# Optimization experiments

Measured on AMD Instinct MI355X. Metric: run time of the kernel, lower is better.

Reference implementation:

```python
import jax, jax.numpy as jnp
import numpy as np

B, T, F, U, L = 64, 700, 3, 400, 3


def setup_inputs() -> dict:
    key = jax.random.key(0)
    ks = jax.random.split(key, 10)
    s = 0.08  # small init to keep gates unsaturated
    return {
        "x": jax.random.normal(ks[0], (B, T, F), jnp.float32),
        "Wx0": jax.random.normal(ks[1], (F, 4 * U), jnp.float32) * s,
        "Wx1": jax.random.normal(ks[2], (U, 4 * U), jnp.float32) * s,
        "Wx2": jax.random.normal(ks[3], (U, 4 * U), jnp.float32) * s,
        "Wh": jax.random.normal(ks[4], (L, U, 4 * U), jnp.float32) * s,
        "b": jnp.zeros((L, 4 * U), jnp.float32),
        "pi": jax.random.normal(ks[5], (L, U), jnp.float32) * s,
        "pf": jax.random.normal(ks[6], (L, U), jnp.float32) * s,
        "po": jax.random.normal(ks[7], (L, U), jnp.float32) * s,
        "Wd": jax.random.normal(ks[8], (U, F), jnp.float32) * s,
        "bd": jnp.zeros((F,), jnp.float32),
    }


def _lstm_peephole_layer(x_tbd, Wx, Wh_l, b_l, pi_l, pf_l, po_l):
    """x_tbd: [T, B, D] -> [T, B, U] with peephole LSTM (Graves 2013)."""
    Bsz = x_tbd.shape[1]
    Uu = Wh_l.shape[0]
    # Precompute the input contribution for all timesteps in one GEMM.
    xp = jnp.einsum("tbd,dk->tbk", x_tbd, Wx) + b_l  # [T, B, 4U]

    def step(carry, zt):
        h, c = carry
        z = zt + h @ Wh_l  # [B, 4U]
        zi, zf, zg, zo = jnp.split(z, 4, axis=-1)
        i = jax.nn.sigmoid(zi + pi_l * c)
        f = jax.nn.sigmoid(zf + pf_l * c)
        c_new = f * c + i * jnp.tanh(zg)
        o = jax.nn.sigmoid(zo + po_l * c_new)
        h_new = o * jnp.tanh(c_new)
        return (h_new, c_new), h_new

    init = (jnp.zeros((Bsz, Uu), x_tbd.dtype), jnp.zeros((Bsz, Uu), x_tbd.dtype))
    _, hs = jax.lax.scan(step, init, xp)
    return hs  # [T, B, U]


def reference(x, Wx0, Wx1, Wx2, Wh, b, pi, pf, po, Wd, bd):
    h = jnp.transpose(x, (1, 0, 2))  # [T, B, F]
    for l, Wx in enumerate((Wx0, Wx1, Wx2)):
        h = _lstm_peephole_layer(h, Wx, Wh[l], b[l], pi[l], pf[l], po[l])
    out = jnp.einsum("tbu,uf->tbf", h, Wd) + bd
    return jnp.transpose(out, (1, 0, 2))  # [B, T, F]
```

## Files before the change

kernel.cpp:

```cpp
#include <hip/hip_runtime.h>
#include <hip/hip_fp16.h>
#include <math.h>

#define B_ 64
#define T_ 700
#define U_ 400
#define NF 704
#define CHUNK_DW 256
#define FR_LS 13312

typedef _Float16 half8 __attribute__((ext_vector_type(8)));
typedef float float4v __attribute__((ext_vector_type(4)));

union AFrag { unsigned u[4]; half8 h; };

__device__ __forceinline__ unsigned agloadu(const unsigned* p) {
    return __hip_atomic_load(p, __ATOMIC_RELAXED, __HIP_MEMORY_SCOPE_AGENT);
}
__device__ __forceinline__ void agstoreu(unsigned* p, unsigned v) {
    __hip_atomic_store(p, v, __ATOMIC_RELAXED, __HIP_MEMORY_SCOPE_AGENT);
}
__device__ __forceinline__ float sig_(float v) {
    return __builtin_amdgcn_rcpf(1.f + __expf(-v));
}
__device__ __forceinline__ float tanh_(float v) {
    return 1.f - 2.f * __builtin_amdgcn_rcpf(__expf(2.f * v) + 1.f);
}
__device__ __forceinline__ void waitflag(const unsigned* f, unsigned target) {
    while (agloadu(f) < target) __builtin_amdgcn_s_sleep(2);
}
__device__ __forceinline__ unsigned f16u(float v) {
    union { _Float16 f; unsigned short s; } cv; cv.f = (_Float16)v; return (unsigned)cv.s;
}

template<int DEPTH, int CP>
__global__ void __launch_bounds__(256, 1)
lstm_mfma(const float* __restrict__ x,
          const float* __restrict__ Wx0,
          const float* __restrict__ Wx1,
          const float* __restrict__ Wx2,
          const float* __restrict__ Wh,
          const float* __restrict__ bias,
          const float* __restrict__ pi,
          const float* __restrict__ pf,
          const float* __restrict__ po,
          const float* __restrict__ Wd,
          const float* __restrict__ bd,
          float* __restrict__ out,
          unsigned* __restrict__ ws)
{
    __shared__ alignas(16) _Float16 wlds[26 * 512];
    __shared__ alignas(16) float zlds[4 * 528];
    __shared__ float gc[160];

    const int LW = NF * CP * 32;
    unsigned* F0 = ws;
    unsigned* F1 = F0 + LW;
    unsigned* F2 = F1 + LW;
    unsigned* FO = F2 + LW;
    unsigned* frag0 = ws + (size_t)4 * LW;

    const int blk  = blockIdx.x;
    const int tid  = threadIdx.x;
    const int lane = tid & 63;
    const int wv   = tid >> 6;
    const int cpi  = (blk + wv) & (CP - 1);

    int layer, u0;
    if      (blk < 50)  { layer = 0; u0 = blk * 8; }
    else if (blk < 150) { layer = 1; u0 = (blk - 50) * 4; }
    else if (blk < 250) { layer = 2; u0 = (blk - 150) * 4; }
    else                { layer = 3; u0 = 0; }

    {
        const float* __restrict__ Wxl = (layer == 1) ? Wx1 : Wx2;
        for (int i = tid; i < 26 * 64; i += 256) {
            const int ln = i & 63, ck = i >> 6;
            const int q = ln >> 4, nn = ln & 15;
            float vals[8];
#pragma unroll
            for (int j = 0; j < 8; ++j) {
                const int kc = ck % 13;
                const int k = kc * 32 + q * 8 + j;
                float v = 0.f;
                if (k < 400) {
                    if (layer == 0) {
                        const int col32 = (ck / 13) * 16 + nn;
                        const int gcol = (col32 >> 3) * U_ + u0 + (col32 & 7);
                        v = Wh[(size_t)k * 1600 + gcol];
                    } else if (layer < 3) {
                        const int gcol = (nn >> 2) * U_ + u0 + (nn & 3);
                        v = (ck >= 13) ? Wh[((size_t)layer * U_ + k) * 1600 + gcol]
                                       : Wxl[(size_t)k * 1600 + gcol];
                    } else {
                        if (ck < 13 && nn < 3) v = Wd[k * 3 + nn];
                    }
                }
                vals[j] = v;
            }
#pragma unroll
            for (int j = 0; j < 8; ++j)
                wlds[ck * 512 + ln * 8 + j] = (_Float16)vals[j];
        }
        if (layer == 0) {
            if (tid < 128) {
                const int col32 = tid >> 2, comp = tid & 3;
                const int gcol = (col32 >> 3) * U_ + u0 + (col32 & 7);
                gc[tid] = (comp == 0) ? bias[gcol] : Wx0[(size_t)(comp - 1) * 1600 + gcol];
            } else if (tid < 152) {
                const int idx = tid - 128, ul = idx / 3, j = idx - ul * 3;
                const float* pp = (j == 0) ? pi : (j == 1) ? pf : po;
                gc[tid] = pp[u0 + ul];
            }
        } else if (layer < 3) {
            if (tid < 16) {
                gc[tid] = bias[layer * 1600 + (tid >> 2) * U_ + u0 + (tid & 3)];
            } else if (tid < 28) {
                const int idx = tid - 16, ul = idx / 3, j = idx - ul * 3;
                const float* pp = (j == 0) ? pi : (j == 1) ? pf : po;
                gc[tid] = pp[layer * U_ + u0 + ul];
            }
        } else {
            if (tid < 3) gc[tid] = bd[tid];
        }
    }
    __syncthreads();

    const int wvz   = wv * 528;
    const int b_loc = lane & 15;
    const int quad  = lane >> 4;
    float cst[2] = {0.f, 0.f};

    for (int t = 0; t < T_; ++t) {
        const int sw = t % DEPTH;
        const int sr = (t + DEPTH - 1) % DEPTH;

        float x0, x1, x2;
        if (layer == 0) {
            const size_t xb = (size_t)(wv * 16 + b_loc) * T_ + t;
            x0 = x[xb * 3 + 0]; x1 = x[xb * 3 + 1]; x2 = x[xb * 3 + 2];
        }

        if (lane == 0) {
            if (layer == 0) {
                if (t >= 1) waitflag(F0 + ((t - 1) * CP + cpi) * 32, 50);
                if (wv == 0 && t >= DEPTH) waitflag(F1 + ((t - DEPTH) * CP + cpi) * 32, 100);
            } else if (layer == 1) {
                if (t >= 1) waitflag(F1 + ((t - 1) * CP + cpi) * 32, 100);
            } else if (layer == 2) {
                if (t >= 1) waitflag(F2 + ((t - 1) * CP + cpi) * 32, 100);
            } else {
                waitflag(F2 + (t * CP + cpi) * 32, 100);
            }
        }
        asm volatile("" ::: "memory");

        AFrag aown[13];
        {
            const unsigned* fr = (layer == 3)
                ? frag0 + ((size_t)(2 * DEPTH + sw)) * FR_LS + wv * 3328
                : frag0 + ((size_t)(layer * DEPTH + sr)) * FR_LS + wv * 3328;
#pragma unroll
            for (int kc = 0; kc < 13; ++kc)
#pragma unroll
                for (int d = 0; d < 4; ++d)
                    aown[kc].u[d] = agloadu(fr + kc * 256 + d * 64 + lane);
        }

        AFrag ainp[13];
        if (layer == 1 || layer == 2) {
            if (lane == 0) {
                if (layer == 1) {
                    waitflag(F0 + (t * CP + cpi) * 32, 50);
                    if (wv == 0 && t >= DEPTH) waitflag(F2 + ((t - DEPTH) * CP + cpi) * 32, 100);
                } else {
                    waitflag(F1 + (t * CP + cpi) * 32, 100);
                    if (wv == 0 && t >= DEPTH) waitflag(FO + ((t - DEPTH) * CP + cpi) * 32, 1);
                }
            }
            asm volatile("" ::: "memory");
            const unsigned* fr = frag0 + ((size_t)((layer - 1) * DEPTH + sw)) * FR_LS + wv * 3328;
#pragma unroll
            for (int kc = 0; kc < 13; ++kc)
#pragma unroll
                for (int d = 0; d < 4; ++d)
                    ainp[kc].u[d] = agloadu(fr + kc * 256 + d * 64 + lane);
        }

        if (layer == 0) {
            float4v acc0 = {0.f, 0.f, 0.f, 0.f}, acc1 = {0.f, 0.f, 0.f, 0.f};
#pragma unroll
            for (int kc = 0; kc < 13; ++kc) {
                const half8 w0 = *(const half8*)&wlds[kc * 512 + lane * 8];
                const half8 w1 = *(const half8*)&wlds[(13 + kc) * 512 + lane * 8];
                acc0 = __builtin_amdgcn_mfma_f32_16x16x32_f16(aown[kc].h, w0, acc0, 0, 0, 0);
                acc1 = __builtin_amdgcn_mfma_f32_16x16x32_f16(aown[kc].h, w1, acc1, 0, 0, 0);
            }
#pragma unroll
            for (int r = 0; r < 4; ++r) {
                zlds[wvz + (quad * 4 + r) * 33 + b_loc] = acc0[r];
                zlds[wvz + (quad * 4 + r) * 33 + 16 + b_loc] = acc1[r];
            }
        } else if (layer < 3) {
            float4v acc = {0.f, 0.f, 0.f, 0.f};
#pragma unroll
            for (int kc = 0; kc < 13; ++kc) {
                const half8 wA = *(const half8*)&wlds[kc * 512 + lane * 8];
                const half8 wB = *(const half8*)&wlds[(13 + kc) * 512 + lane * 8];
                acc = __builtin_amdgcn_mfma_f32_16x16x32_f16(ainp[kc].h, wA, acc, 0, 0, 0);
                acc = __builtin_amdgcn_mfma_f32_16x16x32_f16(aown[kc].h, wB, acc, 0, 0, 0);
            }
#pragma unroll
            for (int r = 0; r < 4; ++r)
                zlds[wvz + (quad * 4 + r) * 33 + b_loc] = acc[r];
        } else {
            float4v acc = {0.f, 0.f, 0.f, 0.f};
#pragma unroll
            for (int kc = 0; kc < 13; ++kc) {
                const half8 w0 = *(const half8*)&wlds[kc * 512 + lane * 8];
                acc = __builtin_amdgcn_mfma_f32_16x16x32_f16(aown[kc].h, w0, acc, 0, 0, 0);
            }
            if (b_loc < 3) {
#pragma unroll
                for (int r = 0; r < 4; ++r)
                    out[((size_t)(wv * 16 + quad * 4 + r) * T_ + t) * 3 + b_loc] = acc[r] + gc[b_loc];
            }
        }
        __syncthreads();

        if (layer == 0) {
            unsigned* fr_dst = frag0 + ((size_t)(0 * DEPTH + sw)) * FR_LS + wv * 3328;
#pragma unroll
            for (int q = 0; q < 2; ++q) {
                const int ul = q * 4 + quad;
                float z[4];
#pragma unroll
                for (int g = 0; g < 4; ++g) {
                    const int gb = (g * 8 + ul) * 4;
                    z[g] = zlds[wvz + b_loc * 33 + g * 8 + ul]
                         + gc[gb + 0] + x0 * gc[gb + 1] + x1 * gc[gb + 2] + x2 * gc[gb + 3];
                }
                const float cp = cst[q];
                const float ig = sig_(z[0] + gc[128 + ul * 3 + 0] * cp);
                const float fg = sig_(z[1] + gc[128 + ul * 3 + 1] * cp);
                const float cn = fg * cp + ig * tanh_(z[2]);
                const float og = sig_(z[3] + gc[128 + ul * 3 + 2] * cn);
                cst[q] = cn;
                const float hv = og * tanh_(cn);
                const float pv = __shfl_xor(hv, 16, 64);
                if ((quad & 1) == 0) {
                    const unsigned pw_ = f16u(hv) | (f16u(pv) << 16);
                    const int u = u0 + ul;
                    agstoreu(fr_dst + (u >> 5) * 256 + ((u & 7) >> 1) * 64
                                    + ((u >> 3) & 3) * 16 + b_loc, pw_);
                }
            }
        } else if (layer < 3) {
            unsigned* fr_dst = frag0 + ((size_t)(layer * DEPTH + sw)) * FR_LS + wv * 3328;
            const int ul = quad;
            float z[4];
#pragma unroll
            for (int g = 0; g < 4; ++g)
                z[g] = zlds[wvz + b_loc * 33 + g * 4 + ul] + gc[g * 4 + ul];
            const float cp = cst[0];
            const float ig = sig_(z[0] + gc[16 + ul * 3 + 0] * cp);
            const float fg = sig_(z[1] + gc[16 + ul * 3 + 1] * cp);
            const float cn = fg * cp + ig * tanh_(z[2]);
            const float og = sig_(z[3] + gc[16 + ul * 3 + 2] * cn);
            cst[0] = cn;
            const float hv = og * tanh_(cn);
            const float pv = __shfl_xor(hv, 16, 64);
            if ((ul & 1) == 0) {
                const unsigned pw_ = f16u(hv) | (f16u(pv) << 16);
                const int u = u0 + ul;
                agstoreu(fr_dst + (u >> 5) * 256 + ((u & 7) >> 1) * 64
                                + ((u >> 3) & 3) * 16 + b_loc, pw_);
            }
        }

        asm volatile("s_waitcnt vmcnt(0)" ::: "memory");
        __syncthreads();
        if (tid < CP) {
            unsigned* f = (layer == 0) ? F0 : (layer == 1) ? F1
                        : (layer == 2) ? F2 : FO;
            __hip_atomic_fetch_add(f + (t * CP + tid) * 32, 1u,
                                   __ATOMIC_RELAXED, __HIP_MEMORY_SCOPE_AGENT);
        }
    }
}

template<int DEPTH, int CP>
static void launch_variant(void* const* d_in, float* out, unsigned* ws, hipStream_t stream) {
    const float* x    = (const float*)d_in[0];
    const float* Wx0  = (const float*)d_in[1];
    const float* Wx1  = (const float*)d_in[2];
    const float* Wx2  = (const float*)d_in[3];
    const float* Wh   = (const float*)d_in[4];
    const float* bias = (const float*)d_in[5];
    const float* pi   = (const float*)d_in[6];
    const float* pf   = (const float*)d_in[7];
    const float* po   = (const float*)d_in[8];
    const float* Wd   = (const float*)d_in[9];
    const float* bd   = (const float*)d_in[10];
    void* args[] = { (void*)&x, (void*)&Wx0, (void*)&Wx1, (void*)&Wx2, (void*)&Wh,
                     (void*)&bias, (void*)&pi, (void*)&pf, (void*)&po,
                     (void*)&Wd, (void*)&bd, (void*)&out, (void*)&ws };
    hipError_t err = hipLaunchCooperativeKernel((void*)lstm_mfma<DEPTH, CP>,
                                                dim3(251), dim3(256), args, 0, stream);
    if (err != hipSuccess)
        hipLaunchKernelGGL((lstm_mfma<DEPTH, CP>), dim3(251), dim3(256), 0, stream,
                           x, Wx0, Wx1, Wx2, Wh, bias, pi, pf, po, Wd, bd, out, ws);
}

extern "C" void kernel_launch(void* const* d_in, const int* in_sizes, int n_in,
                              void* d_out, int out_size, void* d_ws, size_t ws_size,
                              hipStream_t stream) {
    float* out = (float*)d_out;
    unsigned* ws = (unsigned*)d_ws;

    auto need = [](int depth, int cp) -> size_t {
        return (size_t)4 * NF * cp * 32 * 4 + (size_t)3 * depth * FR_LS * 4;
    };

    if (ws_size >= need(8, 8)) {
        hipMemsetAsync(d_ws, 0, need(8, 8), stream);
        launch_variant<8, 8>(d_in, out, ws, stream);
    } else if (ws_size >= need(4, 4)) {
        hipMemsetAsync(d_ws, 0, need(4, 4), stream);
        launch_variant<4, 4>(d_in, out, ws, stream);
    } else {
        hipMemsetAsync(d_ws, 0, need(2, 2), stream);
        launch_variant<2, 2>(d_in, out, ws, stream);
    }
}
```

Measured before the change: 3.337 ms.

## Replace same-layer flag waits with parity-bit polling on fragment data

Drops the per-step counter flag wait for a layer's own previous hidden state. The LSM of each stored fp16 value now carries a parity bit derived from the step index, and readers poll the fragment buffers until every word shows the expected parity. Pad words are written by edge blocks so the whole buffer carries parity, and the buffers are initialised to 0xFF. The aim is to remove a flag round-trip on the recurrent critical path. The cost is one bit of precision in h and extra polling reloads, and correctness depends on relaxed atomics keeping the parity and the data consistent.

```diff
diff --git a/kernel.cpp b/kernel.cpp
--- a/kernel.cpp
+++ b/kernel.cpp
@@ -6,7 +6,6 @@
 #define T_ 700
 #define U_ 400
 #define NF 704
-#define CHUNK_DW 256
 #define FR_LS 13312
 
 typedef _Float16 half8 __attribute__((ext_vector_type(8)));
@@ -33,21 +32,48 @@
     union { _Float16 f; unsigned short s; } cv; cv.f = (_Float16)v; return (unsigned)cv.s;
 }
 
+__device__ __forceinline__ void pollfrag13(const unsigned* __restrict__ base,
+                                           const unsigned par,
+                                           AFrag* __restrict__ a, const int lane)
+{
+    {
+        const unsigned* pp = base + (lane % 13) * 256 + ((lane * 37) & 255);
+        while (!__all((int)(((agloadu(pp) ^ par) & 1u) == 0u)))
+            __builtin_amdgcn_s_sleep(3);
+    }
+    unsigned pend = 0x1FFFu;
+    do {
+#pragma unroll
+        for (int ck = 0; ck < 13; ++ck) if ((pend >> ck) & 1) {
+#pragma unroll
+            for (int d = 0; d < 4; ++d)
+                a[ck].u[d] = agloadu(base + ck * 256 + d * 64 + lane);
+        }
+#pragma unroll
+        for (int ck = 0; ck < 13; ++ck) if ((pend >> ck) & 1) {
+            const unsigned m = (a[ck].u[0] ^ par) | (a[ck].u[1] ^ par)
+                             | (a[ck].u[2] ^ par) | (a[ck].u[3] ^ par);
+            if (__all((int)((m & 1u) == 0u))) pend &= ~(1u << ck);
+        }
+        if (pend) __builtin_amdgcn_s_sleep(3);
+    } while (pend);
+}
+
 template<int DEPTH, int CP>
 __global__ void __launch_bounds__(256, 1)
-lstm_mfma(const float* __restrict__ x,
-          const float* __restrict__ Wx0,
-          const float* __restrict__ Wx1,
-          const float* __restrict__ Wx2,
-          const float* __restrict__ Wh,
-          const float* __restrict__ bias,
-          const float* __restrict__ pi,
-          const float* __restrict__ pf,
-          const float* __restrict__ po,
-          const float* __restrict__ Wd,
-          const float* __restrict__ bd,
-          float* __restrict__ out,
-          unsigned* __restrict__ ws)
+lstm_mix(const float* __restrict__ x,
+         const float* __restrict__ Wx0,
+         const float* __restrict__ Wx1,
+         const float* __restrict__ Wx2,
+         const float* __restrict__ Wh,
+         const float* __restrict__ bias,
+         const float* __restrict__ pi,
+         const float* __restrict__ pf,
+         const float* __restrict__ po,
+         const float* __restrict__ Wd,
+         const float* __restrict__ bd,
+         float* __restrict__ out,
+         unsigned* __restrict__ ws)
 {
     __shared__ alignas(16) _Float16 wlds[26 * 512];
     __shared__ alignas(16) float zlds[4 * 528];
@@ -71,6 +97,16 @@
     else if (blk < 150) { layer = 1; u0 = (blk - 50) * 4; }
     else if (blk < 250) { layer = 2; u0 = (blk - 150) * 4; }
     else                { layer = 3; u0 = 0; }
+
+    const bool padw = (blk == 49) || (blk == 149) || (blk == 249);
+    int pad_off[2];
+    {
+        const int i0 = tid, i1 = tid + 256;
+        pad_off[0] = (i0 >> 7) * 3328 + 12 * 256 + (((i0 >> 4) & 3) * 64)
+                   + (2 + ((i0 >> 6) & 1)) * 16 + (i0 & 15);
+        pad_off[1] = (i1 >> 7) * 3328 + 12 * 256 + (((i1 >> 4) & 3) * 64)
+                   + (2 + ((i1 >> 6) & 1)) * 16 + (i1 & 15);
+    }
 
     {
         const float* __restrict__ Wxl = (layer == 1) ? Wx1 : Wx2;
@@ -134,6 +170,8 @@
     for (int t = 0; t < T_; ++t) {
         const int sw = t % DEPTH;
         const int sr = (t + DEPTH - 1) % DEPTH;
+        const unsigned pI = (unsigned)((t / DEPTH) & 1);
+        const unsigned pO = (unsigned)(((t - 1) / DEPTH) & 1);
 
         float x0, x1, x2;
         if (layer == 0) {
@@ -143,49 +181,47 @@
 
         if (lane == 0) {
             if (layer == 0) {
-                if (t >= 1) waitflag(F0 + ((t - 1) * CP + cpi) * 32, 50);
                 if (wv == 0 && t >= DEPTH) waitflag(F1 + ((t - DEPTH) * CP + cpi) * 32, 100);
             } else if (layer == 1) {
-                if (t >= 1) waitflag(F1 + ((t - 1) * CP + cpi) * 32, 100);
+                waitflag(F0 + (t * CP + cpi) * 32, 50);
+                if (wv == 0 && t >= DEPTH) waitflag(F2 + ((t - DEPTH) * CP + cpi) * 32, 100);
             } else if (layer == 2) {
-                if (t >= 1) waitflag(F2 + ((t - 1) * CP + cpi) * 32, 100);
+                waitflag(F1 + (t * CP + cpi) * 32, 100);
+                if (wv == 0 && t >= DEPTH) waitflag(FO + ((t - DEPTH) * CP + cpi) * 32, 1);
             } else {
                 waitflag(F2 + (t * CP + cpi) * 32, 100);
             }
         }
         asm volatile("" ::: "memory");
 
-        AFrag aown[13];
-        {
-            const unsigned* fr = (layer == 3)
-                ? frag0 + ((size_t)(2 * DEPTH + sw)) * FR_LS + wv * 3328
-                : frag0 + ((size_t)(layer * DEPTH + sr)) * FR_LS + wv * 3328;
-#pragma unroll
-            for (int kc = 0; kc < 13; ++kc)
-#pragma unroll
-                for (int d = 0; d < 4; ++d)
-                    aown[kc].u[d] = agloadu(fr + kc * 256 + d * 64 + lane);
-        }
-
         AFrag ainp[13];
         if (layer == 1 || layer == 2) {
-            if (lane == 0) {
-                if (layer == 1) {
-                    waitflag(F0 + (t * CP + cpi) * 32, 50);
-                    if (wv == 0 && t >= DEPTH) waitflag(F2 + ((t - DEPTH) * CP + cpi) * 32, 100);
-                } else {
-                    waitflag(F1 + (t * CP + cpi) * 32, 100);
-                    if (wv == 0 && t >= DEPTH) waitflag(FO + ((t - DEPTH) * CP + cpi) * 32, 1);
-                }
-            }
-            asm volatile("" ::: "memory");
-            const unsigned* fr = frag0 + ((size_t)((layer - 1) * DEPTH + sw)) * FR_LS + wv * 3328;
+            const unsigned* frI = frag0 + (size_t)((layer - 1) * DEPTH + sw) * FR_LS + wv * 3328;
 #pragma unroll
             for (int kc = 0; kc < 13; ++kc)
 #pragma unroll
                 for (int d = 0; d < 4; ++d)
-                    ainp[kc].u[d] = agloadu(fr + kc * 256 + d * 64 + lane);
-        }
+                    ainp[kc].u[d] = agloadu(frI + kc * 256 + d * 64 + lane);
+        }
+
+        AFrag aown[13];
+        if (layer == 3) {
+            const unsigned* frI = frag0 + (size_t)(2 * DEPTH + sw) * FR_LS + wv * 3328;
+#pragma unroll
+            for (int kc = 0; kc < 13; ++kc)
+#pragma unroll
+                for (int d = 0; d < 4; ++d)
+                    aown[kc].u[d] = agloadu(frI + kc * 256 + d * 64 + lane);
+        } else if (t >= 1) {
+            const unsigned* frO = frag0 + (size_t)(layer * DEPTH + sr) * FR_LS + wv * 3328;
+            pollfrag13(frO, pO, aown, lane);
+        } else {
+#pragma unroll
+            for (int kc = 0; kc < 13; ++kc)
+#pragma unroll
+                for (int d = 0; d < 4; ++d) aown[kc].u[d] = 0u;
+        }
+        asm volatile("" ::: "memory");
 
         if (layer == 0) {
             float4v acc0 = {0.f, 0.f, 0.f, 0.f}, acc1 = {0.f, 0.f, 0.f, 0.f};
@@ -228,11 +264,18 @@
         }
         __syncthreads();
 
+        if (padw) {
+            unsigned* fr_dst = frag0 + (size_t)(layer * DEPTH + sw) * FR_LS;
+            agstoreu(fr_dst + pad_off[0], pI);
+            agstoreu(fr_dst + pad_off[1], pI);
+        }
+
         if (layer == 0) {
-            unsigned* fr_dst = frag0 + ((size_t)(0 * DEPTH + sw)) * FR_LS + wv * 3328;
+            unsigned* fr_dst = frag0 + (size_t)(0 * DEPTH + sw) * FR_LS + wv * 3328;
 #pragma unroll
             for (int q = 0; q < 2; ++q) {
                 const int ul = q * 4 + quad;
+                const int ug = u0 + ul;
                 float z[4];
 #pragma unroll
                 for (int g = 0; g < 4; ++g) {
@@ -249,14 +292,14 @@
                 const float hv = og * tanh_(cn);
                 const float pv = __shfl_xor(hv, 16, 64);
                 if ((quad & 1) == 0) {
-                    const unsigned pw_ = f16u(hv) | (f16u(pv) << 16);
-                    const int u = u0 + ul;
+                    const unsigned pw_ = ((f16u(hv) & ~1u) | pI) | (f16u(pv) << 16);
+                    const int u = ug;
                     agstoreu(fr_dst + (u >> 5) * 256 + ((u & 7) >> 1) * 64
                                     + ((u >> 3) & 3) * 16 + b_loc, pw_);
                 }
             }
         } else if (layer < 3) {
-            unsigned* fr_dst = frag0 + ((size_t)(layer * DEPTH + sw)) * FR_LS + wv * 3328;
+            unsigned* fr_dst = frag0 + (size_t)(layer * DEPTH + sw) * FR_LS + wv * 3328;
             const int ul = quad;
             float z[4];
 #pragma unroll
@@ -271,7 +314,7 @@
             const float hv = og * tanh_(cn);
             const float pv = __shfl_xor(hv, 16, 64);
             if ((ul & 1) == 0) {
-                const unsigned pw_ = f16u(hv) | (f16u(pv) << 16);
+                const unsigned pw_ = ((f16u(hv) & ~1u) | pI) | (f16u(pv) << 16);
                 const int u = u0 + ul;
                 agstoreu(fr_dst + (u >> 5) * 256 + ((u & 7) >> 1) * 64
                                 + ((u >> 3) & 3) * 16 + b_loc, pw_);
@@ -305,10 +348,10 @@
     void* args[] = { (void*)&x, (void*)&Wx0, (void*)&Wx1, (void*)&Wx2, (void*)&Wh,
                      (void*)&bias, (void*)&pi, (void*)&pf, (void*)&po,
                      (void*)&Wd, (void*)&bd, (void*)&out, (void*)&ws };
-    hipError_t err = hipLaunchCooperativeKernel((void*)lstm_mfma<DEPTH, CP>,
+    hipError_t err = hipLaunchCooperativeKernel((void*)lstm_mix<DEPTH, CP>,
                                                 dim3(251), dim3(256), args, 0, stream);
     if (err != hipSuccess)
-        hipLaunchKernelGGL((lstm_mfma<DEPTH, CP>), dim3(251), dim3(256), 0, stream,
+        hipLaunchKernelGGL((lstm_mix<DEPTH, CP>), dim3(251), dim3(256), 0, stream,
                            x, Wx0, Wx1, Wx2, Wh, bias, pi, pf, po, Wd, bd, out, ws);
 }
 
@@ -318,18 +361,20 @@
     float* out = (float*)d_out;
     unsigned* ws = (unsigned*)d_ws;
 
-    auto need = [](int depth, int cp) -> size_t {
-        return (size_t)4 * NF * cp * 32 * 4 + (size_t)3 * depth * FR_LS * 4;
-    };
-
-    if (ws_size >= need(8, 8)) {
-        hipMemsetAsync(d_ws, 0, need(8, 8), stream);
+    auto flagbytes = [](int cp) -> size_t { return (size_t)4 * NF * cp * 32 * 4; };
+    auto fragbytes = [](int depth) -> size_t { return (size_t)3 * depth * FR_LS * 4; };
+
+    if (ws_size >= flagbytes(8) + fragbytes(8)) {
+        hipMemsetAsync(d_ws, 0, flagbytes(8), stream);
+        hipMemsetAsync((char*)d_ws + flagbytes(8), 0xFF, fragbytes(8), stream);
         launch_variant<8, 8>(d_in, out, ws, stream);
-    } else if (ws_size >= need(4, 4)) {
-        hipMemsetAsync(d_ws, 0, need(4, 4), stream);
+    } else if (ws_size >= flagbytes(4) + fragbytes(4)) {
+        hipMemsetAsync(d_ws, 0, flagbytes(4), stream);
+        hipMemsetAsync((char*)d_ws + flagbytes(4), 0xFF, fragbytes(4), stream);
         launch_variant<4, 4>(d_in, out, ws, stream);
     } else {
-        hipMemsetAsync(d_ws, 0, need(2, 2), stream);
+        hipMemsetAsync(d_ws, 0, flagbytes(2), stream);
+        hipMemsetAsync((char*)d_ws + flagbytes(2), 0xFF, fragbytes(2), stream);
         launch_variant<2, 2>(d_in, out, ws, stream);
     }
 }
```

New measurement: 2.844 ms. 14.7% less time.
